# Performance work log

Measured on AMD Instinct MI355X. Metric: run time of the kernel, lower is better.

Reference implementation:

```python
import jax, jax.numpy as jnp
import numpy as np

N, E, R, K1, F = 50000, 400000, 1000, 1000, 128
DEPTH, HEADS = 1, 2

def _l2norm(x, axis):
    n = jnp.sqrt(jnp.maximum(jnp.sum(x * x, axis=axis, keepdims=True), 1e-12))
    return x / n

def _segment_softmax(logits, seg, num_segments):
    m = jax.ops.segment_max(logits, seg, num_segments=num_segments)
    e = jnp.exp(logits - m[seg])
    s = jax.ops.segment_sum(e, seg, num_segments=num_segments)
    return e / s[seg]

def setup_inputs() -> dict:
    rng = np.random.RandomState(0)
    # adjacency: nodes 0..K1-1 have exactly one edge (long-tail), rest random rows
    rows = np.concatenate([np.arange(K1), rng.randint(K1, N, size=E - K1)])
    cols = rng.randint(0, N, size=E)
    order = np.lexsort((cols, rows))
    adj = np.stack([rows, cols], axis=1)[order].astype(np.int32)  # [E,2] sorted by row
    self_nodes_idx = np.arange(K1, dtype=np.int32)
    neights_node_idxs = adj[:K1, 1].astype(np.int32)  # neighbor of each degree-1 node
    sparse_indices = np.stack([np.arange(E), rng.randint(0, R, size=E)], axis=1).astype(np.int32)
    sparse_val = (rng.rand(E).astype(np.float32) * 0.5 + 0.5)
    key = jax.random.key(0)
    k = jax.random.split(key, 5)
    return {
        'features': jax.random.normal(k[0], (N, F), jnp.float32),
        'rel_emb': jax.random.normal(k[1], (R, F), jnp.float32),
        'sparse_val': jnp.asarray(sparse_val),
        'attn_kernels': jax.random.normal(k[2], (DEPTH, HEADS, F), jnp.float32) * (1.0 / np.sqrt(F)),
        'proxy': jax.random.normal(k[3], (64, F * (DEPTH + 1)), jnp.float32) * 0.1,
        'gate_kernel': jax.random.normal(k[4], (F * (DEPTH + 1), F * (DEPTH + 1)), jnp.float32) * (1.0 / np.sqrt(F * (DEPTH + 1))),
        'adj_indices': jnp.asarray(adj),
        'sparse_indices': jnp.asarray(sparse_indices),
        'self_nodes_idx': jnp.asarray(self_nodes_idx),
        'neights_node_idxs': jnp.asarray(neights_node_idxs),
    }

def reference(features, rel_emb, sparse_val, attn_kernels, proxy, gate_kernel,
              adj_indices, sparse_indices, self_nodes_idx, neights_node_idxs):
    row = adj_indices[:, 0]
    col = adj_indices[:, 1]
    feats = features  # activation is linear (None)
    outputs = [feats]
    for l in range(DEPTH):
        # per-triple relation embedding: sparse (E,R) @ rel_emb -> (E,F)
        rels_sum = jax.ops.segment_sum(sparse_val[:, None] * rel_emb[sparse_indices[:, 1]],
                                       sparse_indices[:, 0], num_segments=E)
        rels_norm = _l2norm(rels_sum, axis=1)  # l2 normalize rows
        neighs = feats[col]  # [E,F] gather
        # Householder reflection of neighbor features by relation direction
        neighs = neighs - 2.0 * jnp.sum(neighs * rels_norm, axis=1, keepdims=True) * rels_norm
        head_feats = []
        for head in range(HEADS):
            att_logits = rels_sum @ attn_kernels[l, head]  # [E]
            att = _segment_softmax(att_logits, row, N)  # sparse softmax per destination node
            nf = jax.ops.segment_sum(neighs * att[:, None], row, num_segments=N)  # [N,F]
            if head == 1:
                # long-tail fix: degree-1 nodes copy their single neighbor's aggregated feature
                nf = nf.at[self_nodes_idx].set(nf[neights_node_idxs])
            head_feats.append(nf)
        feats = jnp.mean(jnp.stack(head_feats, axis=0), axis=0)
        outputs.append(feats)
    out = jnp.concatenate(outputs, axis=-1)  # [N, F*(DEPTH+1)]
    proxy_att = jax.nn.softmax(_l2norm(out, axis=-1) @ _l2norm(proxy, axis=-1).T, axis=-1)  # [N,64]
    proxy_feature = out - proxy_att @ proxy
    gate = jax.nn.sigmoid(proxy_feature @ gate_kernel)
    return gate * out + (1.0 - gate) * proxy_feature
```

## Files before the change

kernel.cpp:

```cpp
#include <hip/hip_runtime.h>
#include <math.h>

constexpr int N  = 50000;
constexpr int E  = 400000;
constexpr int R  = 1000;
constexpr int K1 = 1000;
constexpr int F  = 128;
constexpr int OUTC = 256;
constexpr int P  = 64;

typedef _Float16 f16x8 __attribute__((ext_vector_type(8)));
typedef _Float16 f16x4 __attribute__((ext_vector_type(4)));
typedef _Float16 f16x2 __attribute__((ext_vector_type(2)));
typedef float f32x4 __attribute__((ext_vector_type(4)));

#if __has_builtin(__builtin_amdgcn_fdot2)
#define FDOT2(a, b, c) __builtin_amdgcn_fdot2((a), (b), (c), false)
#else
#define FDOT2(a, b, c) fmaf((float)(a)[0], (float)(b)[0], fmaf((float)(a)[1], (float)(b)[1], (c)))
#endif

__device__ inline float waveReduceSum(float v) {
#pragma unroll
    for (int m = 32; m >= 1; m >>= 1) v += __shfl_xor(v, m, 64);
    return v;
}

constexpr int B_FEATSH = 3125;
constexpr int B_REL    = 250;
constexpr int B_SEG    = 1563;
constexpr int B_PSC    = 16;
constexpr int B_PGF    = 64;

__global__ __launch_bounds__(256) void prep_a(
        const float* __restrict__ feats, const float* __restrict__ rel_emb,
        const float* __restrict__ attn,  const float* __restrict__ proxy,
        const float* __restrict__ G,     const int* __restrict__ adj,
        _Float16* __restrict__ featsH,   _Float16* __restrict__ relnormH,
        float* __restrict__ dotr, int* __restrict__ nstart, int* __restrict__ nend,
        float* __restrict__ pscale, float* __restrict__ PGf) {
    int b = blockIdx.x, tid = threadIdx.x;
    if (b < B_FEATSH) {
        int idx = b * 256 + tid;
        float4 x0 = ((const float4*)feats)[2 * idx];
        float4 x1 = ((const float4*)feats)[2 * idx + 1];
        f16x8 h;
        h[0] = (_Float16)x0.x; h[1] = (_Float16)x0.y;
        h[2] = (_Float16)x0.z; h[3] = (_Float16)x0.w;
        h[4] = (_Float16)x1.x; h[5] = (_Float16)x1.y;
        h[6] = (_Float16)x1.z; h[7] = (_Float16)x1.w;
        ((f16x8*)featsH)[idx] = h;
    } else if (b < B_FEATSH + B_REL) {
        int r = (b - B_FEATSH) * 4 + (tid >> 6);
        int lane = tid & 63;
        float2 v  = ((const float2*)(rel_emb + (size_t)r * F))[lane];
        float2 a0 = ((const float2*)attn)[lane];
        float2 a1 = ((const float2*)attn)[64 + lane];
        float ss = waveReduceSum(v.x * v.x + v.y * v.y);
        float d0 = waveReduceSum(v.x * a0.x + v.y * a0.y);
        float d1 = waveReduceSum(v.x * a1.x + v.y * a1.y);
        float sc = rsqrtf(fmaxf(ss, 1e-12f));
        f16x2 h; h[0] = (_Float16)(v.x * sc); h[1] = (_Float16)(v.y * sc);
        ((f16x2*)(relnormH + (size_t)r * F))[lane] = h;
        if (lane == 0) { dotr[2 * r] = d0; dotr[2 * r + 1] = d1; }
    } else if (b < B_FEATSH + B_REL + B_SEG) {
        int e = (b - B_FEATSH - B_REL) * 256 + tid;
        if (e < E) {
            int lane = tid & 63;
            int row = ((const int2*)adj)[e].x;
            int prev = __shfl_up(row, 1, 64);
            if (lane == 0) prev = (e > 0) ? ((const int2*)adj)[e - 1].x : -1;
            int nxt = __shfl_down(row, 1, 64);
            if (lane == 63 && e + 1 < E) nxt = ((const int2*)adj)[e + 1].x;
            if (prev != row) {
                nstart[row] = e;
                for (int rr = prev + 1; rr < row; ++rr) { nstart[rr] = e; nend[rr] = e; }
            }
            if (e == E - 1) {
                nend[row] = E;
                for (int rr = row + 1; rr < N; ++rr) { nstart[rr] = E; nend[rr] = E; }
            } else if (nxt != row) {
                nend[row] = e + 1;
            }
        }
    } else if (b < B_FEATSH + B_REL + B_SEG + B_PSC) {
        int j = (b - B_FEATSH - B_REL - B_SEG) * 4 + (tid >> 6);
        int lane = tid & 63;
        float4 p = ((const float4*)(proxy + (size_t)j * OUTC))[lane];
        float ss = waveReduceSum(p.x * p.x + p.y * p.y + p.z * p.z + p.w * p.w);
        if (lane == 0) pscale[j] = rsqrtf(fmaxf(ss, 1e-12f));
    } else {
        int p = b - (B_FEATSH + B_REL + B_SEG + B_PSC);
        int c = tid;
        float s = 0.f;
        for (int k = 0; k < OUTC; ++k)
            s = fmaf(proxy[(size_t)p * OUTC + k], G[(size_t)k * OUTC + c], s);
        PGf[(size_t)p * OUTC + c] = s;
    }
}

constexpr int NB_NODE = N / 4;
constexpr int NB_FRAG = 56;

__global__ __launch_bounds__(256) void node_frag(
        const _Float16* __restrict__ featsH,
        const _Float16* __restrict__ relnormH,
        const float* __restrict__ dotr,
        const int* __restrict__ adj,
        const int* __restrict__ sidx,
        const float* __restrict__ val,
        const int* __restrict__ nstart,
        const int* __restrict__ nend,
        const float* __restrict__ G,
        const float* __restrict__ proxy,
        const float* __restrict__ pscale,
        const float* __restrict__ PGf,
        _Float16* __restrict__ nf0,
        _Float16* __restrict__ nf1,
        f16x8* __restrict__ Gh, f16x8* __restrict__ pnH,
        f16x8* __restrict__ pxH, f16x8* __restrict__ pgH) {
    if (blockIdx.x >= NB_NODE) {
        int u = (blockIdx.x - NB_NODE) * 4 + (threadIdx.x >> 6);
        int L = threadIdx.x & 63;
        int q = L >> 4, m = L & 15;
        f16x8 h;
        if (u < 128) {
            int kk = u >> 4, cg = u & 15;
            int n = cg * 16 + m;
#pragma unroll
            for (int j = 0; j < 8; ++j)
                h[j] = (_Float16)G[(size_t)(kk * 32 + q * 8 + j) * OUTC + n];
            Gh[(size_t)u * 64 + L] = h;
        } else if (u < 160) {
            int idx = u - 128;
            int kk = idx >> 2, w = idx & 3;
            int n = w * 16 + m;
            float sc = pscale[n];
#pragma unroll
            for (int j = 0; j < 8; ++j)
                h[j] = (_Float16)(proxy[(size_t)n * OUTC + kk * 32 + q * 8 + j] * sc);
            pnH[(size_t)idx * 64 + L] = h;
        } else if (u < 192) {
            int idx = u - 160;
            int kk = idx >> 4, cg = idx & 15;
            int n = cg * 16 + m;
#pragma unroll
            for (int j = 0; j < 8; ++j)
                h[j] = (_Float16)proxy[(size_t)(kk * 32 + q * 8 + j) * OUTC + n];
            pxH[(size_t)idx * 64 + L] = h;
        } else {
            int idx = u - 192;
            int kk = idx >> 4, cg = idx & 15;
            int n = cg * 16 + m;
#pragma unroll
            for (int j = 0; j < 8; ++j)
                h[j] = (_Float16)(-PGf[(size_t)(kk * 32 + q * 8 + j) * OUTC + n]);
            pgH[(size_t)idx * 64 + L] = h;
        }
        return;
    }
    int n = blockIdx.x * 4 + (threadIdx.x >> 6);
    int lane = threadIdx.x & 63;
    int g = lane >> 4, gl = lane & 15;
    int start = nstart[n], end = nend[n];
    const int2* adj2 = (const int2*)adj;
    const int2* sx2  = (const int2*)sidx;
    float A0[8], A1[8];
#pragma unroll
    for (int j = 0; j < 8; ++j) { A0[j] = 0.f; A1[j] = 0.f; }
    float s0 = 0.f, s1 = 0.f;
    for (int e = start + g; e < end; e += 8) {
        int eB = e + 4;
        bool hasB = (eB < end);
        int eBc = hasB ? eB : e;
        int colA = adj2[e].y,   colB = adj2[eBc].y;
        int relA = sx2[e].y,    relB = sx2[eBc].y;
        float vA = val[e],      vB = val[eBc];
        float2 drA = ((const float2*)dotr)[relA];
        float2 drB = ((const float2*)dotr)[relB];
        float wA0 = __expf(vA * drA.x), wA1 = __expf(vA * drA.y);
        float wB0 = hasB ? __expf(vB * drB.x) : 0.f;
        float wB1 = hasB ? __expf(vB * drB.y) : 0.f;
        s0 += wA0 + wB0; s1 += wA1 + wB1;
        f16x8 fAv = ((const f16x8*)(featsH   + (size_t)colA * F))[gl];
        f16x8 rAv = ((const f16x8*)(relnormH + (size_t)relA * F))[gl];
        f16x8 fBv = ((const f16x8*)(featsH   + (size_t)colB * F))[gl];
        f16x8 rBv = ((const f16x8*)(relnormH + (size_t)relB * F))[gl];
        const f16x2* fA2 = (const f16x2*)&fAv;
        const f16x2* rA2 = (const f16x2*)&rAv;
        const f16x2* fB2 = (const f16x2*)&fBv;
        const f16x2* rB2 = (const f16x2*)&rBv;
        float pdA = 0.f, pdB = 0.f;
#pragma unroll
        for (int j = 0; j < 4; ++j) {
            pdA = FDOT2(fA2[j], rA2[j], pdA);
            pdB = FDOT2(fB2[j], rB2[j], pdB);
        }
        pdA += __shfl_xor(pdA, 1, 64); pdB += __shfl_xor(pdB, 1, 64);
        pdA += __shfl_xor(pdA, 2, 64); pdB += __shfl_xor(pdB, 2, 64);
        pdA += __shfl_xor(pdA, 4, 64); pdB += __shfl_xor(pdB, 4, 64);
        pdA += __shfl_xor(pdA, 8, 64); pdB += __shfl_xor(pdB, 8, 64);
        _Float16 tAh = (_Float16)(2.f * pdA), tBh = (_Float16)(2.f * pdB);
        f16x2 tA2; tA2[0] = tAh; tA2[1] = tAh;
        f16x2 tB2; tB2[0] = tBh; tB2[1] = tBh;
#pragma unroll
        for (int j = 0; j < 4; ++j) {
            f16x2 rxA = fA2[j] - tA2 * rA2[j];
            f16x2 rxB = fB2[j] - tB2 * rB2[j];
            float x0 = (float)rxA[0], x1 = (float)rxA[1];
            float y0 = (float)rxB[0], y1 = (float)rxB[1];
            A0[2*j]   = fmaf(wA0, x0, A0[2*j]);   A0[2*j]   = fmaf(wB0, y0, A0[2*j]);
            A0[2*j+1] = fmaf(wA0, x1, A0[2*j+1]); A0[2*j+1] = fmaf(wB0, y1, A0[2*j+1]);
            A1[2*j]   = fmaf(wA1, x0, A1[2*j]);   A1[2*j]   = fmaf(wB1, y0, A1[2*j]);
            A1[2*j+1] = fmaf(wA1, x1, A1[2*j+1]); A1[2*j+1] = fmaf(wB1, y1, A1[2*j+1]);
        }
    }
#pragma unroll
    for (int j = 0; j < 8; ++j) {
        A0[j] += __shfl_xor(A0[j], 16, 64); A0[j] += __shfl_xor(A0[j], 32, 64);
        A1[j] += __shfl_xor(A1[j], 16, 64); A1[j] += __shfl_xor(A1[j], 32, 64);
    }
    s0 += __shfl_xor(s0, 16, 64); s0 += __shfl_xor(s0, 32, 64);
    s1 += __shfl_xor(s1, 16, 64); s1 += __shfl_xor(s1, 32, 64);
    float i0 = (s0 > 0.f) ? 1.f / s0 : 0.f;
    float i1 = (s1 > 0.f) ? 1.f / s1 : 0.f;
    if (g == 0) {
        f16x8 h0, h1;
#pragma unroll
        for (int j = 0; j < 8; ++j) {
            h0[j] = (_Float16)(A0[j] * i0);
            h1[j] = (_Float16)(A1[j] * i1);
        }
        ((f16x8*)(nf0 + (size_t)n * F))[gl] = h0;
        ((f16x8*)(nf1 + (size_t)n * F))[gl] = h1;
    }
}

__global__ __launch_bounds__(512, 6) void proxy_gate(
        const _Float16* __restrict__ featsH,
        const _Float16* __restrict__ nf0,
        const _Float16* __restrict__ nf1,
        const int* __restrict__ neigh,
        const f16x8* __restrict__ pnH,
        const f16x8* __restrict__ pxH,
        const f16x8* __restrict__ Gh,
        const f16x8* __restrict__ pgH,
        float* __restrict__ out) {
    constexpr int LDA  = 68;
    constexpr int LDAH = 72;
    __shared__ __align__(16) f16x8 outH[16 * 64];
    __shared__ __align__(16) float attL[32 * LDA];
    __shared__ __align__(16) _Float16 attH[32 * LDAH];
    __shared__ float scaleL[32];
    int tid = threadIdx.x;
    int w = tid >> 6, lane = tid & 63;
    int quad = lane >> 4, m = lane & 15;
    size_t row0 = (size_t)blockIdx.x * 32;

    {
        int bm = tid >> 4, gl = tid & 15;
        int n = (int)row0 + bm;
        float ss;
        f16x8 h1, h2;
        if (n < N) {
            ss = 0.f;
            h1 = ((const f16x8*)(featsH + (size_t)n * F))[gl];
#pragma unroll
            for (int j = 0; j < 8; ++j) { float x = (float)h1[j]; ss += x * x; }
            int sel = (n < K1) ? neigh[n] : n;
            f16x8 a  = ((const f16x8*)(nf0 + (size_t)n   * F))[gl];
            f16x8 b2 = ((const f16x8*)(nf1 + (size_t)sel * F))[gl];
#pragma unroll
            for (int j = 0; j < 8; ++j) {
                float v = 0.5f * ((float)a[j] + (float)b2[j]);
                h2[j] = (_Float16)v;
                ss += v * v;
            }
        } else {
#pragma unroll
            for (int j = 0; j < 8; ++j) { h1[j] = (_Float16)0.f; h2[j] = (_Float16)0.f; }
            ss = 1.f;
        }
        int t = bm >> 4, r16 = bm & 15;
        outH[(t * 8 +     (gl >> 2)) * 64 + (gl & 3) * 16 + r16] = h1;
        outH[(t * 8 + 4 + (gl >> 2)) * 64 + (gl & 3) * 16 + r16] = h2;
        ss += __shfl_xor(ss, 1, 64); ss += __shfl_xor(ss, 2, 64);
        ss += __shfl_xor(ss, 4, 64); ss += __shfl_xor(ss, 8, 64);
        if (gl == 0) scaleL[bm] = rsqrtf(fmaxf(ss, 1e-12f));
    }
    __syncthreads();

    int tl = w >> 2;
    int pg = w & 3;
    f32x4 lacc = (f32x4){0,0,0,0};
    f32x4 zacc[2][2];
#pragma unroll
    for (int t = 0; t < 2; ++t)
#pragma unroll
        for (int c = 0; c < 2; ++c) zacc[t][c] = (f32x4){0,0,0,0};
#pragma unroll
    for (int kk = 0; kk < 8; ++kk) {
        f16x8 pb  = pnH[(size_t)(kk * 4 + pg) * 64 + lane];
        f16x8 gb0 = Gh[(size_t)(kk * 16 + w)     * 64 + lane];
        f16x8 gb1 = Gh[(size_t)(kk * 16 + w + 8) * 64 + lane];
        f16x8 a0 = outH[(0 * 8 + kk) * 64 + lane];
        f16x8 a1 = outH[(1 * 8 + kk) * 64 + lane];
        f16x8 at = tl ? a1 : a0;
        lacc       = __builtin_amdgcn_mfma_f32_16x16x32_f16(at, pb,  lacc,       0, 0, 0);
        zacc[0][0] = __builtin_amdgcn_mfma_f32_16x16x32_f16(a0, gb0, zacc[0][0], 0, 0, 0);
        zacc[0][1] = __builtin_amdgcn_mfma_f32_16x16x32_f16(a0, gb1, zacc[0][1], 0, 0, 0);
        zacc[1][0] = __builtin_amdgcn_mfma_f32_16x16x32_f16(a1, gb0, zacc[1][0], 0, 0, 0);
        zacc[1][1] = __builtin_amdgcn_mfma_f32_16x16x32_f16(a1, gb1, zacc[1][1], 0, 0, 0);
    }
#pragma unroll
    for (int i = 0; i < 4; ++i) {
        int r = tl * 16 + quad * 4 + i;
        attL[r * LDA + pg * 16 + m] = lacc[i] * scaleL[r];
    }
    __syncthreads();

#pragma unroll
    for (int i = 0; i < 4; ++i) {
        int r = 4 * w + i;
        float e = __expf(attL[r * LDA + lane]);
        float s = waveReduceSum(e);
        attH[r * LDAH + lane] = (_Float16)(e / s);
    }
    __syncthreads();

    f32x4 qacc[2][2];
#pragma unroll
    for (int t = 0; t < 2; ++t)
#pragma unroll
        for (int c = 0; c < 2; ++c) qacc[t][c] = (f32x4){0,0,0,0};
#pragma unroll
    for (int kk = 0; kk < 2; ++kk) {
        f16x8 a[2];
#pragma unroll
        for (int t = 0; t < 2; ++t)
            a[t] = *(const f16x8*)&attH[(t * 16 + m) * LDAH + kk * 32 + quad * 8];
#pragma unroll
        for (int cgi = 0; cgi < 2; ++cgi) {
            int cg = w + 8 * cgi;
            f16x8 bx = pxH[(size_t)(kk * 16 + cg) * 64 + lane];
            f16x8 bg = pgH[(size_t)(kk * 16 + cg) * 64 + lane];
#pragma unroll
            for (int t = 0; t < 2; ++t) {
                qacc[t][cgi] = __builtin_amdgcn_mfma_f32_16x16x32_f16(a[t], bx, qacc[t][cgi], 0, 0, 0);
                zacc[t][cgi] = __builtin_amdgcn_mfma_f32_16x16x32_f16(a[t], bg, zacc[t][cgi], 0, 0, 0);
            }
        }
    }

    const _Float16* outHs = (const _Float16*)outH;
#pragma unroll
    for (int t = 0; t < 2; ++t) {
        if ((int)row0 + t * 16 >= N) continue;
#pragma unroll
        for (int cgi = 0; cgi < 2; ++cgi) {
            int cg = w + 8 * cgi;
            int c = cg * 16 + m;
            int kkc = cg >> 1;
            int qc = ((cg & 1) << 1) | (m >> 3);
            int j = m & 7;
#pragma unroll
            for (int i = 0; i < 4; ++i) {
                int r15 = quad * 4 + i;
                float ov = (float)outHs[(((t * 8 + kkc) * 64 + qc * 16 + r15) << 3) + j];
                float gate = 1.f / (1.f + __expf(-zacc[t][cgi][i]));
                size_t n = row0 + t * 16 + r15;
                out[n * OUTC + c] = ov - (1.f - gate) * qacc[t][cgi][i];
            }
        }
    }
}

extern "C" void kernel_launch(void* const* d_in, const int* in_sizes, int n_in,
                              void* d_out, int out_size, void* d_ws, size_t ws_size,
                              hipStream_t stream) {
    const float* features   = (const float*)d_in[0];
    const float* rel_emb    = (const float*)d_in[1];
    const float* sparse_val = (const float*)d_in[2];
    const float* attn       = (const float*)d_in[3];
    const float* proxy      = (const float*)d_in[4];
    const float* gateK      = (const float*)d_in[5];
    const int*   adj        = (const int*)d_in[6];
    const int*   sidx       = (const int*)d_in[7];
    const int*   neigh      = (const int*)d_in[9];
    float* out = (float*)d_out;

    char* ws = (char*)d_ws;
    size_t off = 0;
    auto alloc = [&](size_t bytes) -> void* {
        void* p = ws + off;
        off += (bytes + 255) & ~(size_t)255;
        return p;
    };
    _Float16* relnormH = (_Float16*)alloc((size_t)R * F * 2);
    float*    dotr     = (float*)alloc((size_t)R * 2 * 4);
    float*    pscale   = (float*)alloc((size_t)P * 4);
    float*    PGf      = (float*)alloc((size_t)P * OUTC * 4);
    f16x8*    Gh       = (f16x8*)alloc((size_t)128 * 64 * 16);
    f16x8*    pnH      = (f16x8*)alloc((size_t)32 * 64 * 16);
    f16x8*    pxH      = (f16x8*)alloc((size_t)32 * 64 * 16);
    f16x8*    pgH      = (f16x8*)alloc((size_t)32 * 64 * 16);
    _Float16* featsH   = (_Float16*)alloc((size_t)N * F * 2);
    int*      nstart   = (int*)alloc((size_t)N * 4);
    int*      nend     = (int*)alloc((size_t)N * 4);
    _Float16* nf0      = (_Float16*)alloc((size_t)N * F * 2);
    _Float16* nf1      = (_Float16*)alloc((size_t)N * F * 2);

    prep_a<<<B_FEATSH + B_REL + B_SEG + B_PSC + B_PGF, 256, 0, stream>>>(
        features, rel_emb, attn, proxy, gateK, adj,
        featsH, relnormH, dotr, nstart, nend, pscale, PGf);
    node_frag<<<NB_NODE + NB_FRAG, 256, 0, stream>>>(
        featsH, relnormH, dotr, adj, sidx, sparse_val, nstart, nend,
        gateK, proxy, pscale, PGf,
        nf0, nf1, Gh, pnH, pxH, pgH);
    proxy_gate<<<(N + 31) / 32, 512, 0, stream>>>(
        featsH, nf0, nf1, neigh, pnH, pxH, Gh, pgH, out);
}
```

Baseline: 174.4 us.

## Process 64 rows per block in proxy_gate to reuse weight fragments

The proxy_gate kernel now handles four 16-row tiles per block instead of two, halving the grid. Each wave reuses the loaded gate-kernel and proxy B-fragments across twice as many MFMA tiles, cutting global weight traffic per row. This raises register and LDS use per block, so launch bounds drop from 6 to 4 blocks per CU, and the wave-per-row softmax now covers 8 rows per wave.

```diff
diff --git a/kernel.cpp b/kernel.cpp
--- a/kernel.cpp
+++ b/kernel.cpp
@@ -236,7 +236,7 @@
     }
 }
 
-__global__ __launch_bounds__(512, 6) void proxy_gate(
+__global__ __launch_bounds__(512, 4) void proxy_gate(
         const _Float16* __restrict__ featsH,
         const _Float16* __restrict__ nf0,
         const _Float16* __restrict__ nf1,
@@ -246,56 +246,61 @@
         const f16x8* __restrict__ Gh,
         const f16x8* __restrict__ pgH,
         float* __restrict__ out) {
+    constexpr int RT   = 4;
     constexpr int LDA  = 68;
     constexpr int LDAH = 72;
-    __shared__ __align__(16) f16x8 outH[16 * 64];
-    __shared__ __align__(16) float attL[32 * LDA];
-    __shared__ __align__(16) _Float16 attH[32 * LDAH];
-    __shared__ float scaleL[32];
+    __shared__ __align__(16) f16x8 outH[RT * 8 * 64];
+    __shared__ __align__(16) float attL[RT * 16 * LDA];
+    __shared__ __align__(16) _Float16 attH[RT * 16 * LDAH];
+    __shared__ float scaleL[RT * 16];
     int tid = threadIdx.x;
     int w = tid >> 6, lane = tid & 63;
     int quad = lane >> 4, m = lane & 15;
-    size_t row0 = (size_t)blockIdx.x * 32;
+    size_t row0 = (size_t)blockIdx.x * (RT * 16);
 
     {
-        int bm = tid >> 4, gl = tid & 15;
-        int n = (int)row0 + bm;
-        float ss;
-        f16x8 h1, h2;
-        if (n < N) {
-            ss = 0.f;
-            h1 = ((const f16x8*)(featsH + (size_t)n * F))[gl];
-#pragma unroll
-            for (int j = 0; j < 8; ++j) { float x = (float)h1[j]; ss += x * x; }
-            int sel = (n < K1) ? neigh[n] : n;
-            f16x8 a  = ((const f16x8*)(nf0 + (size_t)n   * F))[gl];
-            f16x8 b2 = ((const f16x8*)(nf1 + (size_t)sel * F))[gl];
-#pragma unroll
-            for (int j = 0; j < 8; ++j) {
-                float v = 0.5f * ((float)a[j] + (float)b2[j]);
-                h2[j] = (_Float16)v;
-                ss += v * v;
+        int bm0 = tid >> 4, gl = tid & 15;
+#pragma unroll
+        for (int half = 0; half < 2; ++half) {
+            int bm = bm0 + 32 * half;
+            int n = (int)row0 + bm;
+            float ss;
+            f16x8 h1, h2;
+            if (n < N) {
+                ss = 0.f;
+                h1 = ((const f16x8*)(featsH + (size_t)n * F))[gl];
+#pragma unroll
+                for (int j = 0; j < 8; ++j) { float x = (float)h1[j]; ss += x * x; }
+                int sel = (n < K1) ? neigh[n] : n;
+                f16x8 a  = ((const f16x8*)(nf0 + (size_t)n   * F))[gl];
+                f16x8 b2 = ((const f16x8*)(nf1 + (size_t)sel * F))[gl];
+#pragma unroll
+                for (int j = 0; j < 8; ++j) {
+                    float v = 0.5f * ((float)a[j] + (float)b2[j]);
+                    h2[j] = (_Float16)v;
+                    ss += v * v;
+                }
+            } else {
+#pragma unroll
+                for (int j = 0; j < 8; ++j) { h1[j] = (_Float16)0.f; h2[j] = (_Float16)0.f; }
+                ss = 1.f;
             }
-        } else {
-#pragma unroll
-            for (int j = 0; j < 8; ++j) { h1[j] = (_Float16)0.f; h2[j] = (_Float16)0.f; }
-            ss = 1.f;
-        }
-        int t = bm >> 4, r16 = bm & 15;
-        outH[(t * 8 +     (gl >> 2)) * 64 + (gl & 3) * 16 + r16] = h1;
-        outH[(t * 8 + 4 + (gl >> 2)) * 64 + (gl & 3) * 16 + r16] = h2;
-        ss += __shfl_xor(ss, 1, 64); ss += __shfl_xor(ss, 2, 64);
-        ss += __shfl_xor(ss, 4, 64); ss += __shfl_xor(ss, 8, 64);
-        if (gl == 0) scaleL[bm] = rsqrtf(fmaxf(ss, 1e-12f));
+            int t = bm >> 4, r16 = bm & 15;
+            outH[(t * 8 +     (gl >> 2)) * 64 + (gl & 3) * 16 + r16] = h1;
+            outH[(t * 8 + 4 + (gl >> 2)) * 64 + (gl & 3) * 16 + r16] = h2;
+            ss += __shfl_xor(ss, 1, 64); ss += __shfl_xor(ss, 2, 64);
+            ss += __shfl_xor(ss, 4, 64); ss += __shfl_xor(ss, 8, 64);
+            if (gl == 0) scaleL[bm] = rsqrtf(fmaxf(ss, 1e-12f));
+        }
     }
     __syncthreads();
 
-    int tl = w >> 2;
+    int tl0 = w >> 2;
     int pg = w & 3;
-    f32x4 lacc = (f32x4){0,0,0,0};
-    f32x4 zacc[2][2];
-#pragma unroll
-    for (int t = 0; t < 2; ++t)
+    f32x4 lacc[2] = {(f32x4){0,0,0,0}, (f32x4){0,0,0,0}};
+    f32x4 zacc[RT][2];
+#pragma unroll
+    for (int t = 0; t < RT; ++t)
 #pragma unroll
         for (int c = 0; c < 2; ++c) zacc[t][c] = (f32x4){0,0,0,0};
 #pragma unroll
@@ -305,39 +310,51 @@
         f16x8 gb1 = Gh[(size_t)(kk * 16 + w + 8) * 64 + lane];
         f16x8 a0 = outH[(0 * 8 + kk) * 64 + lane];
         f16x8 a1 = outH[(1 * 8 + kk) * 64 + lane];
-        f16x8 at = tl ? a1 : a0;
-        lacc       = __builtin_amdgcn_mfma_f32_16x16x32_f16(at, pb,  lacc,       0, 0, 0);
+        f16x8 a2 = outH[(2 * 8 + kk) * 64 + lane];
+        f16x8 a3 = outH[(3 * 8 + kk) * 64 + lane];
+        f16x8 aL0 = tl0 ? a1 : a0;
+        f16x8 aL1 = tl0 ? a3 : a2;
+        lacc[0]    = __builtin_amdgcn_mfma_f32_16x16x32_f16(aL0, pb,  lacc[0],    0, 0, 0);
+        lacc[1]    = __builtin_amdgcn_mfma_f32_16x16x32_f16(aL1, pb,  lacc[1],    0, 0, 0);
         zacc[0][0] = __builtin_amdgcn_mfma_f32_16x16x32_f16(a0, gb0, zacc[0][0], 0, 0, 0);
         zacc[0][1] = __builtin_amdgcn_mfma_f32_16x16x32_f16(a0, gb1, zacc[0][1], 0, 0, 0);
         zacc[1][0] = __builtin_amdgcn_mfma_f32_16x16x32_f16(a1, gb0, zacc[1][0], 0, 0, 0);
         zacc[1][1] = __builtin_amdgcn_mfma_f32_16x16x32_f16(a1, gb1, zacc[1][1], 0, 0, 0);
-    }
-#pragma unroll
-    for (int i = 0; i < 4; ++i) {
-        int r = tl * 16 + quad * 4 + i;
-        attL[r * LDA + pg * 16 + m] = lacc[i] * scaleL[r];
+        zacc[2][0] = __builtin_amdgcn_mfma_f32_16x16x32_f16(a2, gb0, zacc[2][0], 0, 0, 0);
+        zacc[2][1] = __builtin_amdgcn_mfma_f32_16x16x32_f16(a2, gb1, zacc[2][1], 0, 0, 0);
+        zacc[3][0] = __builtin_amdgcn_mfma_f32_16x16x32_f16(a3, gb0, zacc[3][0], 0, 0, 0);
+        zacc[3][1] = __builtin_amdgcn_mfma_f32_16x16x32_f16(a3, gb1, zacc[3][1], 0, 0, 0);
+    }
+#pragma unroll
+    for (int u = 0; u < 2; ++u) {
+        int tile = tl0 + 2 * u;
+#pragma unroll
+        for (int i = 0; i < 4; ++i) {
+            int r = tile * 16 + quad * 4 + i;
+            attL[r * LDA + pg * 16 + m] = lacc[u][i] * scaleL[r];
+        }
     }
     __syncthreads();
 
 #pragma unroll
-    for (int i = 0; i < 4; ++i) {
-        int r = 4 * w + i;
+    for (int i = 0; i < 8; ++i) {
+        int r = 8 * w + i;
         float e = __expf(attL[r * LDA + lane]);
         float s = waveReduceSum(e);
         attH[r * LDAH + lane] = (_Float16)(e / s);
     }
     __syncthreads();
 
-    f32x4 qacc[2][2];
-#pragma unroll
-    for (int t = 0; t < 2; ++t)
+    f32x4 qacc[RT][2];
+#pragma unroll
+    for (int t = 0; t < RT; ++t)
 #pragma unroll
         for (int c = 0; c < 2; ++c) qacc[t][c] = (f32x4){0,0,0,0};
 #pragma unroll
     for (int kk = 0; kk < 2; ++kk) {
-        f16x8 a[2];
-#pragma unroll
-        for (int t = 0; t < 2; ++t)
+        f16x8 a[RT];
+#pragma unroll
+        for (int t = 0; t < RT; ++t)
             a[t] = *(const f16x8*)&attH[(t * 16 + m) * LDAH + kk * 32 + quad * 8];
 #pragma unroll
         for (int cgi = 0; cgi < 2; ++cgi) {
@@ -345,7 +362,7 @@
             f16x8 bx = pxH[(size_t)(kk * 16 + cg) * 64 + lane];
             f16x8 bg = pgH[(size_t)(kk * 16 + cg) * 64 + lane];
 #pragma unroll
-            for (int t = 0; t < 2; ++t) {
+            for (int t = 0; t < RT; ++t) {
                 qacc[t][cgi] = __builtin_amdgcn_mfma_f32_16x16x32_f16(a[t], bx, qacc[t][cgi], 0, 0, 0);
                 zacc[t][cgi] = __builtin_amdgcn_mfma_f32_16x16x32_f16(a[t], bg, zacc[t][cgi], 0, 0, 0);
             }
@@ -354,7 +371,7 @@
 
     const _Float16* outHs = (const _Float16*)outH;
 #pragma unroll
-    for (int t = 0; t < 2; ++t) {
+    for (int t = 0; t < RT; ++t) {
         if ((int)row0 + t * 16 >= N) continue;
 #pragma unroll
         for (int cgi = 0; cgi < 2; ++cgi) {
@@ -417,6 +434,6 @@
         featsH, relnormH, dotr, adj, sidx, sparse_val, nstart, nend,
         gateK, proxy, pscale, PGf,
         nf0, nf1, Gh, pnH, pxH, pgH);
-    proxy_gate<<<(N + 31) / 32, 512, 0, stream>>>(
+    proxy_gate<<<(N + 63) / 64, 512, 0, stream>>>(
         featsH, nf0, nf1, neigh, pnH, pxH, Gh, pgH, out);
 }
```

New measurement: 171.1 us, median of 3. About the same (-1.9%).
